# Performance work log

Measured on AMD Instinct MI355X. Metric: run time of the kernel, lower is better.

## Reference

```python
import jax, jax.numpy as jnp
import numpy as np

NF, NX, GROUP_SIZE = 8192, 2048, 64
N_GROUPS = NX // GROUP_SIZE  # pad = 0 since NX % GROUP_SIZE == 0


def setup_inputs() -> dict:
    key = jax.random.key(0)
    k1, k2, k3, k4, k5 = jax.random.split(key, 5)
    x = jax.random.normal(k1, (4, 2048, NX), dtype=jnp.float32)
    packed = jax.random.randint(k2, (NF, NX // 2), 0, 256, dtype=jnp.int32)
    scales = jax.random.uniform(k3, (NF, N_GROUPS), dtype=jnp.float32)
    zeros = jax.random.randint(k4, (NF, N_GROUPS), 0, 16, dtype=jnp.int32)
    bias = jax.random.normal(k5, (NF,), dtype=jnp.float32)
    return {"x": x, "packed": packed, "scales": scales, "zeros": zeros, "bias": bias}


def _dequantize(packed, scales, zeros):
    # packed: [nf, nx//2] bytes, two int4 nibbles per byte (low nibble first)
    low = packed & 15
    high = (packed >> 4) & 15
    # interleave: q[:, 0::2] = low, q[:, 1::2] = high
    q = jnp.stack([low, high], axis=-1).reshape(NF, NX).astype(jnp.float32)
    q = q.reshape(NF, N_GROUPS, GROUP_SIZE)
    W = (q - zeros.astype(jnp.float32)[:, :, None]) * scales[:, :, None]
    return W.reshape(NF, NX)  # [nf, nx]


def reference(x, packed, scales, zeros, bias):
    W = _dequantize(packed, scales, zeros).astype(x.dtype)  # [nf, nx]
    size_out = x.shape[:-1] + (NF,)
    out = jnp.matmul(x.reshape(-1, NX), W.T) + bias  # addmm
    return out.reshape(size_out)
```

## Files before the change

### kernel.cpp

```cpp
#include <hip/hip_runtime.h>
#include <stdint.h>

#define NF 8192
#define NX 2048
#define MROWS 8192
#define NGROUPS 32
#define NTILE 64

typedef unsigned short u16;
typedef __bf16 bf16x8 __attribute__((ext_vector_type(8)));
typedef float f32x16 __attribute__((ext_vector_type(16)));

#define AS1 __attribute__((address_space(1)))
#define AS3 __attribute__((address_space(3)))

__device__ __forceinline__ void glds16(const void* g, void* l) {
    __builtin_amdgcn_global_load_lds((AS1 void*)(uintptr_t)g,
                                     (AS3 void*)(uintptr_t)l, 16, 0, 0);
}

__device__ __forceinline__ u16 f2bf(float f) {
    unsigned u = __float_as_uint(f);
    return (u16)((u + 0x7FFFu + ((u >> 16) & 1u)) >> 16);
}

__global__ void dequant_kernel(const int* __restrict__ packed,
                               const float* __restrict__ scales,
                               const int* __restrict__ zeros,
                               uint32_t* __restrict__ W2) {
    int tid = blockIdx.x * blockDim.x + threadIdx.x;
    int f = tid >> 10;
    int i = tid & 1023;
    int g = f * NGROUPS + (i >> 5);
    int p = packed[tid];
    float s = scales[g];
    float z = (float)zeros[g];
    float w0 = ((float)(p & 15) - z) * s;
    float w1 = ((float)((p >> 4) & 15) - z) * s;
    W2[tid] = (uint32_t)f2bf(w0) | ((uint32_t)f2bf(w1) << 16);
}

__global__ void cvt_kernel(const float4* __restrict__ x, ushort4* __restrict__ y) {
    int i = blockIdx.x * blockDim.x + threadIdx.x;
    float4 v = x[i];
    ushort4 o;
    o.x = f2bf(v.x); o.y = f2bf(v.y); o.z = f2bf(v.z); o.w = f2bf(v.w);
    y[i] = o;
}


#define BAR    __builtin_amdgcn_s_barrier()
#define LGKM0  asm volatile("s_waitcnt lgkmcnt(0)" ::: "memory")
#define VMCNT0 asm volatile("s_waitcnt vmcnt(0)" ::: "memory")
#define FENCE  __builtin_amdgcn_sched_barrier(0)

#define LD8(off) (*(const bf16x8*)(smem + (off)))

#define MFMA32(d, va, vb) d = __builtin_amdgcn_mfma_f32_32x32x16_bf16(va, vb, d, 0, 0, 0)

#define RDBANK(aX, bX, BUF, U) do { \
    aX[0] = LD8((BUF) + aOff + (U)); \
    aX[1] = LD8((BUF) + aOff + 2048 + (U)); \
    bX[0] = LD8((BUF) + bOff + (U)); \
    bX[1] = LD8((BUF) + bOff + 2048 + (U)); \
} while (0)

#define MM2(aX, bX) do { \
    MFMA32(acc[0][0], aX[0], bX[0]); \
    MFMA32(acc[0][1], aX[0], bX[1]); \
    MFMA32(acc[1][0], aX[1], bX[0]); \
    MFMA32(acc[1][1], aX[1], bX[1]); \
} while (0)

#define STAGE3(BUF, KOFF) do { \
    glds16(srcA + (KOFF),          smem + (BUF) + t16); \
    glds16(srcA + 524288 + (KOFF), smem + (BUF) + 8192 + t16); \
    glds16(srcB + (KOFF),          smem + (BUF) + 16384 + t16); \
} while (0)

__global__ __launch_bounds__(512, 4)
void gemm_kernel(const u16* __restrict__ A, const u16* __restrict__ B,
                 const float* __restrict__ bias, float* __restrict__ C) {
    __shared__ __align__(16) char smem[49152];

    const int t = threadIdx.x;

    const int bid = blockIdx.x;
    const int xcd = bid & 7;
    const int local = bid >> 3;
    const int super = local >> 7;
    const int r = local & 127;
    const int by = xcd * 4 + super * 2 + (r & 1);
    const int bx = r >> 1;
    const int rowA0 = by * 256;
    const int rowB0 = bx * 128;

    const int t16 = t * 16;
    const int ulog = (t & 7) ^ ((t >> 3) & 7);
    const int urow = 2 * (t >> 3) + (ulog >> 2);
    const int ks16 = (ulog & 3) * 16;
    const char* srcA = (const char*)A + (size_t)(rowA0 + urow) * 4096 + ks16;
    const char* srcB = (const char*)B + (size_t)(rowB0 + urow) * 4096 + ks16;

    const int lane = t & 63;
    const int wv = t >> 6;
    const int wm = wv >> 1;
    const int wn = wv & 1;
    const int l31 = lane & 31;
    const int hi = lane >> 5;
    const int lh = l31 >> 1;
    const int x7 = lh & 7;
    const int ux4 = (l31 & 1) * 4;
    const int u0 = ((ux4 + hi) ^ x7) << 4;
    const int u1 = ((ux4 + 2 + hi) ^ x7) << 4;
    const int aOff = (wm * 32 + lh) * 128;
    const int bOff = 16384 + (wn * 32 + lh) * 128;

    f32x16 acc[2][2];
#pragma unroll
    for (int i = 0; i < 2; ++i)
#pragma unroll
        for (int n = 0; n < 2; ++n)
#pragma unroll
            for (int e = 0; e < 16; ++e) acc[i][n][e] = 0.f;

    bf16x8 aE[2], bE[2], aO[2], bO[2];

    STAGE3(0, 0);
    VMCNT0;

#pragma unroll 1
    for (int T = 0; T < NTILE; ++T) {
        const int bo = (T & 1) * 24576;
        const int so = 24576 - bo;

        FENCE; BAR; FENCE;
        RDBANK(aE, bE, bo, u0);
        if (T + 1 < NTILE) STAGE3(so, (T + 1) * 64);
        FENCE; LGKM0; FENCE;
        RDBANK(aO, bO, bo, u1);
        FENCE;
        __builtin_amdgcn_s_setprio(1);
        MM2(aE, bE);
        __builtin_amdgcn_s_setprio(0);
        FENCE; LGKM0; FENCE;
        __builtin_amdgcn_s_setprio(1);
        MM2(aO, bO);
        __builtin_amdgcn_s_setprio(0);
        FENCE;
        VMCNT0;
    }

    const int col0 = rowB0 + wn * 64 + l31;
    const int row0 = rowA0 + wm * 64 + 4 * hi;
    const float bj0 = bias[col0];
    const float bj1 = bias[col0 + 32];
    float* Cbase = C + col0;
#pragma unroll
    for (int i = 0; i < 2; ++i) {
#pragma unroll
        for (int e = 0; e < 16; ++e) {
            const int row = row0 + i * 32 + (e & 3) + 8 * (e >> 2);
            float* crow = Cbase + (size_t)row * NF;
            __builtin_nontemporal_store(acc[i][0][e] + bj0, crow);
            __builtin_nontemporal_store(acc[i][1][e] + bj1, crow + 32);
        }
    }
}

extern "C" void kernel_launch(void* const* d_in, const int* in_sizes, int n_in,
                              void* d_out, int out_size, void* d_ws, size_t ws_size,
                              hipStream_t stream) {
    const float* x      = (const float*)d_in[0];
    const int* packed   = (const int*)d_in[1];
    const float* scales = (const float*)d_in[2];
    const int* zeros    = (const int*)d_in[3];
    const float* bias   = (const float*)d_in[4];
    float* out = (float*)d_out;

    u16* Wq = (u16*)d_ws;
    u16* Xb = Wq + (size_t)NF * NX;

    dequant_kernel<<<(NF * (NX / 2)) / 256, 256, 0, stream>>>(packed, scales, zeros, (uint32_t*)Wq);
    cvt_kernel<<<(MROWS * NX / 4) / 256, 256, 0, stream>>>((const float4*)x, (ushort4*)Xb);

    gemm_kernel<<<dim3((MROWS / 256) * (NF / 128)), 512, 0, stream>>>(Xb, Wq, bias, out);
}
```

Baseline: 330.0 us.

## Triple-buffer LDS tiles with prefetch distance two and re-swizzled row layout

The GEMM main loop moves from double buffering to a three-stage LDS ring. Tiles are prefetched two K-steps ahead, and each iteration waits with vmcnt(3) instead of draining all outstanding global loads. To keep the fragment reads consistent, the LDS layout now pairs row r with row r+64 in each 128-byte line, and the A/B fragment offsets and swizzles are recomputed to match. The aim is to hide global-to-LDS load latency behind the MFMAs, at the cost of growing LDS from 48KB to 72KB per block, which may lower how many blocks fit on a CU.

```diff
diff --git a/kernel.cpp b/kernel.cpp
--- a/kernel.cpp
+++ b/kernel.cpp
@@ -51,6 +51,7 @@
 
 #define BAR    __builtin_amdgcn_s_barrier()
 #define LGKM0  asm volatile("s_waitcnt lgkmcnt(0)" ::: "memory")
+#define VMCNT3 asm volatile("s_waitcnt vmcnt(3)" ::: "memory")
 #define VMCNT0 asm volatile("s_waitcnt vmcnt(0)" ::: "memory")
 #define FENCE  __builtin_amdgcn_sched_barrier(0)
 
@@ -58,11 +59,11 @@
 
 #define MFMA32(d, va, vb) d = __builtin_amdgcn_mfma_f32_32x32x16_bf16(va, vb, d, 0, 0, 0)
 
-#define RDBANK(aX, bX, BUF, U) do { \
-    aX[0] = LD8((BUF) + aOff + (U)); \
-    aX[1] = LD8((BUF) + aOff + 2048 + (U)); \
-    bX[0] = LD8((BUF) + bOff + (U)); \
-    bX[1] = LD8((BUF) + bOff + 2048 + (U)); \
+#define RDBANK(aX, bX, BUF, UA, UB) do { \
+    aX[0] = LD8((BUF) + aOff + (UA)); \
+    aX[1] = LD8((BUF) + aOff + 4096 + (UA)); \
+    bX[0] = LD8((BUF) + bOff + (UB)); \
+    bX[1] = LD8((BUF) + bOff + 4096 + (UB)); \
 } while (0)
 
 #define MM2(aX, bX) do { \
@@ -81,7 +82,7 @@
 __global__ __launch_bounds__(512, 4)
 void gemm_kernel(const u16* __restrict__ A, const u16* __restrict__ B,
                  const float* __restrict__ bias, float* __restrict__ C) {
-    __shared__ __align__(16) char smem[49152];
+    __shared__ __align__(16) char smem[73728];
 
     const int t = threadIdx.x;
 
@@ -97,7 +98,7 @@
 
     const int t16 = t * 16;
     const int ulog = (t & 7) ^ ((t >> 3) & 7);
-    const int urow = 2 * (t >> 3) + (ulog >> 2);
+    const int urow = (t >> 3) + (ulog >> 2) * 64;
     const int ks16 = (ulog & 3) * 16;
     const char* srcA = (const char*)A + (size_t)(rowA0 + urow) * 4096 + ks16;
     const char* srcB = (const char*)B + (size_t)(rowB0 + urow) * 4096 + ks16;
@@ -108,13 +109,15 @@
     const int wn = wv & 1;
     const int l31 = lane & 31;
     const int hi = lane >> 5;
-    const int lh = l31 >> 1;
-    const int x7 = lh & 7;
-    const int ux4 = (l31 & 1) * 4;
-    const int u0 = ((ux4 + hi) ^ x7) << 4;
-    const int u1 = ((ux4 + 2 + hi) ^ x7) << 4;
-    const int aOff = (wm * 32 + lh) * 128;
-    const int bOff = 16384 + (wn * 32 + lh) * 128;
+    const int xl = l31 & 7;
+    const int am = (wm & 1) * 4;
+    const int bm = wn * 4;
+    const int uA0 = ((am + hi) ^ xl) << 4;
+    const int uA1 = ((am + 2 + hi) ^ xl) << 4;
+    const int uB0 = ((bm + hi) ^ xl) << 4;
+    const int uB1 = ((bm + 2 + hi) ^ xl) << 4;
+    const int aOff = ((wm >> 1) * 64 + l31) * 128;
+    const int bOff = 16384 + l31 * 128;
 
     f32x16 acc[2][2];
 #pragma unroll
@@ -126,19 +129,20 @@
 
     bf16x8 aE[2], bE[2], aO[2], bO[2];
 
-    STAGE3(0, 0);
-    VMCNT0;
+    STAGE3(0,     0);
+    STAGE3(24576, 64);
+    VMCNT3;
+
+    int bufC = 0, bufN = 24576, bufT = 49152;
+    int kOff = 128;
 
 #pragma unroll 1
     for (int T = 0; T < NTILE; ++T) {
-        const int bo = (T & 1) * 24576;
-        const int so = 24576 - bo;
-
         FENCE; BAR; FENCE;
-        RDBANK(aE, bE, bo, u0);
-        if (T + 1 < NTILE) STAGE3(so, (T + 1) * 64);
+        RDBANK(aE, bE, bufC, uA0, uB0);
+        if (T < NTILE - 2) STAGE3(bufT, kOff);
         FENCE; LGKM0; FENCE;
-        RDBANK(aO, bO, bo, u1);
+        RDBANK(aO, bO, bufC, uA1, uB1);
         FENCE;
         __builtin_amdgcn_s_setprio(1);
         MM2(aE, bE);
@@ -148,7 +152,11 @@
         MM2(aO, bO);
         __builtin_amdgcn_s_setprio(0);
         FENCE;
-        VMCNT0;
+        if (T < NTILE - 2) VMCNT3;
+        else if (T < NTILE - 1) VMCNT0;
+
+        const int tmp = bufC; bufC = bufN; bufN = bufT; bufT = tmp;
+        kOff += 64;
     }
 
     const int col0 = rowB0 + wn * 64 + l31;
```

After: 330.0 us. About the same (-0.0%).
